# Performance work log

Hardware: AMD Instinct MI355X
Metric: run time of the kernel (lower is better)

Reference implementation:

```python
import jax, jax.numpy as jnp
import numpy as np

B, T, C, K = 8, 2048, 1024, 128

def setup_inputs() -> dict:
    key = jax.random.key(0)
    k1, k2, k3, k4 = jax.random.split(key, 4)
    scale = 0.02
    return {
        "x": jax.random.normal(k1, (B, T, C), dtype=jnp.float32),
        "Wq": jax.random.normal(k2, (C, K), dtype=jnp.float32) * scale,
        "Wk": jax.random.normal(k3, (C, K), dtype=jnp.float32) * scale,
        "Wv": jax.random.normal(k4, (C, K), dtype=jnp.float32) * scale,
    }

def reference(x, Wq, Wk, Wv):
    # Single-head causal self-attention (ModulUwagi.forward)
    q = jnp.einsum('btc,ck->btk', x, Wq)  # [B,T,K]
    k = jnp.einsum('btc,ck->btk', x, Wk)
    v = jnp.einsum('btc,ck->btk', x, Wv)
    hd = q.shape[-1]
    wei = jnp.einsum('btk,bsk->bts', q, k) * (hd ** -0.5)  # [B,T,T]
    causal = jnp.tril(jnp.ones((x.shape[1], x.shape[1]), dtype=bool))
    wei = jnp.where(causal, wei, -jnp.inf)
    wei = jax.nn.softmax(wei, axis=-1)
    out = jnp.einsum('bts,bsk->btk', wei, v)  # [B,T,K]
    return out
```

## Files before the change

kernel.cpp:

```cpp
#include <hip/hip_runtime.h>
#include <cmath>

#define Bn 8
#define Tn 2048
#define Cn 1024
#define Kn 128

typedef __attribute__((ext_vector_type(8))) short short8;
typedef __attribute__((ext_vector_type(4))) float f32x4;
typedef unsigned short u16;
typedef unsigned int u32;

#define NEGINF (-__builtin_huge_valf())

__device__ __forceinline__ u16 f2b(float f) {
    u32 u = __float_as_uint(f);
    u32 r = (u + 0x7FFFu + ((u >> 16) & 1u)) >> 16;
    return (u16)r;
}
__device__ __forceinline__ float b2f(u16 v) {
    u32 u = ((u32)v) << 16;
    return __uint_as_float(u);
}
__device__ __forceinline__ u32 cvtpk(float lo, float hi) {
    u32 r;
    asm("v_cvt_pk_bf16_f32 %0, %1, %2" : "=v"(r) : "v"(lo), "v"(hi));
    return r;
}

__device__ __forceinline__ void load_lds16(const u16* g, u16* l) {
    __builtin_amdgcn_global_load_lds(
        (const __attribute__((address_space(1))) u32*)(g),
        (__attribute__((address_space(3))) u32*)(l), 16, 0, 0);
}

__global__ __launch_bounds__(256)
void prep_kernel(const float* __restrict__ Wq, const float* __restrict__ Wk,
                 const float* __restrict__ Wv, u16* __restrict__ Wt)
{
    int id = blockIdx.x * 256 + threadIdx.x;
    int w   = id >> 15;
    int rem = id & 32767;
    int c   = rem >> 5;
    int n4  = (rem & 31) << 2;
    const float* W = (w == 0) ? Wq : (w == 1) ? Wk : Wv;
    float4 v = *(const float4*)(W + (size_t)c * Kn + n4);
    u16* dst = Wt + (size_t)w * Kn * Cn;
    dst[(size_t)(n4 + 0) * Cn + c] = f2b(v.x);
    dst[(size_t)(n4 + 1) * Cn + c] = f2b(v.y);
    dst[(size_t)(n4 + 2) * Cn + c] = f2b(v.z);
    dst[(size_t)(n4 + 3) * Cn + c] = f2b(v.w);
}

__global__ __launch_bounds__(256)
void proj3_kernel(const float* __restrict__ x, const u16* __restrict__ Wt,
                  u16* __restrict__ qkv)
{
    const int bid = blockIdx.x;
    const int g8  = bid >> 3, xr = bid & 7;
    const int w   = g8 % 3;
    const int rt  = (g8 / 3) * 8 + xr;
    const u16* wtg = Wt + (size_t)w * Kn * Cn;
    u16* outp = qkv + (size_t)w * Bn * Tn * Kn;
    const int row0 = rt * 128;
    const int tid  = threadIdx.x;
    const int lane = tid & 63;
    const int wid  = tid >> 6;
    const int l15  = lane & 15, lh = lane >> 4;
    const int m0 = (wid >> 1) * 64, n0 = (wid & 1) * 64;

    __shared__ u16 lds[32768];

    auto stageW = [&](int kk, int buf) {
        #pragma unroll
        for (int i = 0; i < 4; ++i) {
            int u = tid + i * 256;
            int n = u >> 3, c8 = u & 7;
            load_lds16(wtg + (size_t)n * Cn + kk + ((c8 ^ (n & 7)) << 3),
                       lds + 16384 + buf * 8192 + u * 8);
        }
    };
    auto loadX = [&](int kk, float4* xr4) {
        #pragma unroll
        for (int i = 0; i < 4; ++i) {
            int u = tid + i * 256;
            int r = u >> 3, c8 = u & 7;
            const float* s = x + (size_t)(row0 + r) * Cn + kk + c8 * 8;
            xr4[2 * i]     = *(const float4*)(s);
            xr4[2 * i + 1] = *(const float4*)(s + 4);
        }
    };
    auto writeX = [&](int buf, const float4* xr4) {
        u16* dst = lds + buf * 8192;
        #pragma unroll
        for (int i = 0; i < 4; ++i) {
            int u = tid + i * 256;
            int r = u >> 3, c8 = u & 7;
            uint4 pk;
            pk.x = cvtpk(xr4[2 * i].x,     xr4[2 * i].y);
            pk.y = cvtpk(xr4[2 * i].z,     xr4[2 * i].w);
            pk.z = cvtpk(xr4[2 * i + 1].x, xr4[2 * i + 1].y);
            pk.w = cvtpk(xr4[2 * i + 1].z, xr4[2 * i + 1].w);
            *(uint4*)(dst + r * 64 + ((c8 ^ (r & 7)) << 3)) = pk;
        }
    };

    f32x4 acc[4][4];
    #pragma unroll
    for (int i = 0; i < 4; ++i)
        #pragma unroll
        for (int j = 0; j < 4; ++j) acc[i][j] = (f32x4){0.f, 0.f, 0.f, 0.f};

    float4 xcur[8];
    loadX(0, xcur);
    stageW(0, 0);
    writeX(0, xcur);

    for (int step = 0; step < 16; ++step) {
        const int buf = step & 1;
        __syncthreads();
        const bool nxt = (step < 15);
        float4 xnext[8];
        if (nxt) {
            loadX((step + 1) * 64, xnext);
            stageW((step + 1) * 64, buf ^ 1);
        }
        const u16* Xb = lds + buf * 8192;
        const u16* Wb = lds + 16384 + buf * 8192;
        #pragma unroll
        for (int kc = 0; kc < 2; ++kc) {
            short8 af[4], bf[4];
            #pragma unroll
            for (int mg = 0; mg < 4; ++mg) {
                int row = m0 + mg * 16 + l15;
                int ch  = (kc * 4 + lh) ^ (row & 7);
                af[mg] = *(const short8*)(Xb + row * 64 + ch * 8);
            }
            #pragma unroll
            for (int ng = 0; ng < 4; ++ng) {
                int n  = n0 + ng * 16 + l15;
                int ch = (kc * 4 + lh) ^ (n & 7);
                bf[ng] = *(const short8*)(Wb + n * 64 + ch * 8);
            }
            #pragma unroll
            for (int mg = 0; mg < 4; ++mg)
                #pragma unroll
                for (int ng = 0; ng < 4; ++ng)
                    acc[mg][ng] = __builtin_amdgcn_mfma_f32_16x16x32_bf16(
                        af[mg], bf[ng], acc[mg][ng], 0, 0, 0);
        }
        if (nxt) writeX(buf ^ 1, xnext);
    }

    #pragma unroll
    for (int mg = 0; mg < 4; ++mg)
        #pragma unroll
        for (int ng = 0; ng < 4; ++ng)
            #pragma unroll
            for (int r = 0; r < 4; ++r) {
                int m = row0 + m0 + mg * 16 + lh * 4 + r;
                int n = n0 + ng * 16 + l15;
                outp[(size_t)m * Kn + n] = f2b(acc[mg][ng][r]);
            }
}

__device__ const int g_job_qi[32] = {0, 1,1, 2,2,2, 3,3,3,3, 4,4,4,4,
                                     5,5,5,5,5, 6,6,6,6,6,6, 7,7,7,7,7,7,7};
__device__ const int g_sup_b[32] = {0, 0,4, 0,4,8, 0,4,8,12, 0,5,10,15,
                                    0,4,9,14,19, 0,4,9,14,18,23, 0,4,9,13,18,22,27};
__device__ const int g_sup_e[32] = {4, 4,8, 4,8,12, 4,8,12,16, 5,10,15,20,
                                    4,9,14,19,24, 4,9,14,18,23,28, 4,9,13,18,22,27,32};

__global__ __launch_bounds__(512, 2)
void attn_kernel(const u16* __restrict__ qg_, const u16* __restrict__ kg_,
                 const u16* __restrict__ vg_, u16* __restrict__ pO,
                 float* __restrict__ pM, float* __restrict__ pL)
{
    const int b   = blockIdx.x;
    const int job = blockIdx.y;
    const int qi  = g_job_qi[job];
    const int sb  = g_sup_b[job], se = g_sup_e[job];

    const u16* qw = qg_ + (size_t)b * Tn * Kn;
    const u16* kw = kg_ + (size_t)b * Tn * Kn;
    const u16* vw = vg_ + (size_t)b * Tn * Kn;

    const int tid  = threadIdx.x;
    const int lane = tid & 63;
    const int wid  = tid >> 6;
    const int l15  = lane & 15, lh = lane >> 4;

    const int q0 = qi * 256 + wid * 32;
    const int qmax_w = q0 + 31;

    __shared__ u16 lds[32768];

    short8 qf[2][4];
    #pragma unroll
    for (int g = 0; g < 2; ++g)
        #pragma unroll
        for (int kc = 0; kc < 4; ++kc)
            qf[g][kc] = *(const short8*)(qw + (size_t)(q0 + g * 16 + l15) * Kn
                                         + kc * 32 + lh * 8);

    f32x4 acc[8][2];
    #pragma unroll
    for (int dt = 0; dt < 8; ++dt)
        #pragma unroll
        for (int g = 0; g < 2; ++g) acc[dt][g] = (f32x4){0.f, 0.f, 0.f, 0.f};
    float m_g[2] = {NEGINF, NEGINF}, l_g[2] = {0.f, 0.f};

    const float scale = 0.08838834764831843f;

    auto stageK = [&](int sup, int buf) {
        const u16* src = kw + (size_t)sup * 64 * Kn;
        u16* dst = lds + buf * 8192;
        #pragma unroll
        for (int i = 0; i < 2; ++i) {
            int u = wid * 128 + i * 64 + lane;
            int row = u >> 4;
            int c16 = (u & 15) ^ (row & 7);
            load_lds16(src + (size_t)row * Kn + c16 * 8,
                       dst + (size_t)(wid * 128 + i * 64) * 8);
        }
    };
    auto loadV = [&](int sup, uint4* vr) {
        const u16* src = vw + (size_t)sup * 64 * Kn;
        #pragma unroll
        for (int r = 0; r < 2; ++r) {
            int s  = tid & 63;
            int u8 = (tid >> 6) + 8 * r;
            vr[r] = *(const uint4*)(src + (size_t)s * Kn + u8 * 8);
        }
    };
    auto writeV = [&](int buf, const uint4* vr) {
        u16* dst = lds + 16384 + buf * 8192;
        #pragma unroll
        for (int r = 0; r < 2; ++r) {
            int s  = tid & 63;
            int u8 = (tid >> 6) + 8 * r;
            const u16* e = (const u16*)&vr[r];
            #pragma unroll
            for (int j = 0; j < 8; ++j) {
                int d = u8 * 8 + j;
                dst[d * 64 + (((s >> 3) ^ j) << 3) + (s & 7)] = e[j];
            }
        }
    };

    uint4 vreg[2];
    stageK(sb, 0);
    loadV(sb, vreg);
    writeV(0, vreg);

    for (int sup = sb; sup < se; ++sup) {
        const int cur = (sup - sb) & 1;
        __syncthreads();
        const bool have_next = (sup + 1 < se);
        if (have_next) {
            stageK(sup + 1, cur ^ 1);
            loadV(sup + 1, vreg);
        }
        if (sup * 64 <= qmax_w) {
            const u16* Kb = lds + cur * 8192;
            const u16* Vb = lds + 16384 + cur * 8192;
            f32x4 sf[4][2];
            #pragma unroll
            for (int mt = 0; mt < 4; ++mt)
                #pragma unroll
                for (int g = 0; g < 2; ++g) sf[mt][g] = (f32x4){0.f,0.f,0.f,0.f};
            #pragma unroll
            for (int kc = 0; kc < 4; ++kc) {
                short8 a[4];
                #pragma unroll
                for (int mt = 0; mt < 4; ++mt) {
                    int row = mt * 16 + l15;
                    int ch  = (kc * 4 + lh) ^ (row & 7);
                    a[mt] = *(const short8*)(Kb + row * 128 + ch * 8);
                }
                #pragma unroll
                for (int mt = 0; mt < 4; ++mt)
                    #pragma unroll
                    for (int g = 0; g < 2; ++g)
                        sf[mt][g] = __builtin_amdgcn_mfma_f32_16x16x32_bf16(
                            a[mt], qf[g][kc], sf[mt][g], 0, 0, 0);
            }
            const int sbase = sup * 64;
            u32 upk[2][4][2];
            float alpha_g[2];
            #pragma unroll
            for (int g = 0; g < 2; ++g) {
                const int qg = q0 + g * 16 + l15;
                float pv[16];
                float pm = NEGINF;
                #pragma unroll
                for (int mt = 0; mt < 4; ++mt)
                    #pragma unroll
                    for (int r = 0; r < 4; ++r) {
                        int sg = sbase + mt * 16 + lh * 4 + r;
                        float vv = sf[mt][g][r] * scale;
                        vv = (sg > qg) ? NEGINF : vv;
                        pv[mt * 4 + r] = vv;
                        pm = fmaxf(pm, vv);
                    }
                pm = fmaxf(pm, __shfl_xor(pm, 16));
                pm = fmaxf(pm, __shfl_xor(pm, 32));
                float mn  = fmaxf(m_g[g], pm);
                float mns = (mn == NEGINF) ? 0.f : mn;
                float al  = __expf(m_g[g] - mns);
                m_g[g] = mn;
                alpha_g[g] = al;
                float ps = 0.f;
                #pragma unroll
                for (int i = 0; i < 16; ++i) { pv[i] = __expf(pv[i] - mns); ps += pv[i]; }
                ps += __shfl_xor(ps, 16);
                ps += __shfl_xor(ps, 32);
                l_g[g] = l_g[g] * al + ps;
                #pragma unroll
                for (int mt = 0; mt < 4; ++mt)
                    #pragma unroll
                    for (int h = 0; h < 2; ++h)
                        upk[g][mt][h] = (u32)f2b(pv[mt * 4 + 2 * h])
                                      | ((u32)f2b(pv[mt * 4 + 2 * h + 1]) << 16);
            }
            #pragma unroll
            for (int dt = 0; dt < 8; ++dt)
                #pragma unroll
                for (int g = 0; g < 2; ++g)
                    acc[dt][g] *= alpha_g[g];
            #pragma unroll
            for (int ks = 0; ks < 2; ++ks) {
                short8 pf[2];
                #pragma unroll
                for (int g = 0; g < 2; ++g) {
                    union { u32 w[4]; short8 v; } uu;
                    #pragma unroll
                    for (int hp = 0; hp < 4; ++hp) {
                        int srcLane = l15 + 16 * ((lh & 1) * 2 + (hp >> 1));
                        u32 vA = __shfl(upk[g][2 * ks][hp & 1], srcLane, 64);
                        u32 vB = __shfl(upk[g][2 * ks + 1][hp & 1], srcLane, 64);
                        uu.w[hp] = (lh < 2) ? vA : vB;
                    }
                    pf[g] = uu.v;
                }
                #pragma unroll
                for (int dt = 0; dt < 8; ++dt) {
                    int d  = dt * 16 + l15;
                    int ch = (ks * 4 + lh) ^ (d & 7);
                    short8 av = *(const short8*)(Vb + d * 64 + ch * 8);
                    #pragma unroll
                    for (int g = 0; g < 2; ++g)
                        acc[dt][g] = __builtin_amdgcn_mfma_f32_16x16x32_bf16(
                            av, pf[g], acc[dt][g], 0, 0, 0);
                }
            }
        }
        if (have_next) writeV(cur ^ 1, vreg);
    }

    const size_t slotrow = ((size_t)b * 32 + job) * 256 + wid * 32;
    #pragma unroll
    for (int g = 0; g < 2; ++g) {
        size_t row = slotrow + g * 16 + l15;
        #pragma unroll
        for (int dt = 0; dt < 8; ++dt) {
            ushort4 o = { f2b(acc[dt][g][0]), f2b(acc[dt][g][1]),
                          f2b(acc[dt][g][2]), f2b(acc[dt][g][3]) };
            *(ushort4*)(pO + row * 128 + dt * 16 + lh * 4) = o;
        }
        if (lh == 0) {
            pM[row] = m_g[g];
            pL[row] = l_g[g];
        }
    }
}

__device__ const int g_cnt[8] = {1, 2, 3, 4, 4, 5, 6, 7};
__device__ const int g_s0[8]  = {0, 1, 3, 6, 10, 14, 19, 25};

__global__ __launch_bounds__(256)
void merge_kernel(const u16* __restrict__ pO, const float* __restrict__ pM,
                  const float* __restrict__ pL, float* __restrict__ out)
{
    const int bid = blockIdx.x;
    const int b   = bid >> 8;
    const int rem = bid & 255;
    const int qi  = rem >> 5;
    const int rg  = rem & 31;
    const int c = g_cnt[qi], s0 = g_s0[qi];
    const int tid = threadIdx.x;
    const int r8 = tid >> 5;
    const int dg = tid & 31;

    const int row = rg * 8 + r8;
    const size_t base = ((size_t)b * 32 + s0) * 256 + row;

    float mv[8];
    float M = NEGINF;
    #pragma unroll
    for (int i = 0; i < 8; ++i)
        if (i < c) { mv[i] = pM[base + (size_t)i * 256]; M = fmaxf(M, mv[i]); }
    float L = 0.f, w[8];
    #pragma unroll
    for (int i = 0; i < 8; ++i)
        if (i < c) {
            float e = __expf(mv[i] - M);
            L += pL[base + (size_t)i * 256] * e;
            w[i] = e;
        }
    const float invL = 1.f / L;

    float4 o = {0.f, 0.f, 0.f, 0.f};
    #pragma unroll
    for (int i = 0; i < 8; ++i)
        if (i < c) {
            ushort4 p = *(const ushort4*)(pO + (base + (size_t)i * 256) * 128 + dg * 4);
            float wi = w[i] * invL;
            o.x = fmaf(wi, b2f(p.x), o.x);
            o.y = fmaf(wi, b2f(p.y), o.y);
            o.z = fmaf(wi, b2f(p.z), o.z);
            o.w = fmaf(wi, b2f(p.w), o.w);
        }
    *(float4*)(out + ((size_t)b * Tn + qi * 256 + row) * Kn + dg * 4) = o;
}

extern "C" void kernel_launch(void* const* d_in, const int* in_sizes, int n_in,
                              void* d_out, int out_size, void* d_ws, size_t ws_size,
                              hipStream_t stream)
{
    const float* x  = (const float*)d_in[0];
    const float* Wq = (const float*)d_in[1];
    const float* Wk = (const float*)d_in[2];
    const float* Wv = (const float*)d_in[3];
    float* out = (float*)d_out;

    u16* ws = (u16*)d_ws;
    const size_t btk = (size_t)Bn * Tn * Kn;
    u16* q  = ws;
    u16* k  = ws + btk;
    u16* v  = ws + 2 * btk;
    u16* Wt = ws + 3 * btk;
    u16* pO = ws + 3 * btk + 393216;
    float* pM = (float*)(pO + (size_t)8388608);
    float* pL = pM + 65536;

    prep_kernel<<<384, 256, 0, stream>>>(Wq, Wk, Wv, Wt);
    proj3_kernel<<<384, 256, 0, stream>>>(x, Wt, ws);
    attn_kernel<<<dim3(Bn, 32), 512, 0, stream>>>(q, k, v, pO, pM, pL);
    merge_kernel<<<2048, 256, 0, stream>>>(pO, pM, pL, out);
}
```

Baseline: 71.80 us.

## Deepen projection pipeline with two-stage X register prefetch and manual waitcnt barriers

```diff
diff --git a/kernel.cpp b/kernel.cpp
--- a/kernel.cpp
+++ b/kernel.cpp
@@ -53,7 +53,7 @@
 }
 
 __global__ __launch_bounds__(256)
-void proj3_kernel(const float* __restrict__ x, const u16* __restrict__ Wt,
+void proj4_kernel(const float* __restrict__ x, const u16* __restrict__ Wt,
                   u16* __restrict__ qkv)
 {
     const int bid = blockIdx.x;
@@ -111,20 +111,7 @@
         #pragma unroll
         for (int j = 0; j < 4; ++j) acc[i][j] = (f32x4){0.f, 0.f, 0.f, 0.f};
 
-    float4 xcur[8];
-    loadX(0, xcur);
-    stageW(0, 0);
-    writeX(0, xcur);
-
-    for (int step = 0; step < 16; ++step) {
-        const int buf = step & 1;
-        __syncthreads();
-        const bool nxt = (step < 15);
-        float4 xnext[8];
-        if (nxt) {
-            loadX((step + 1) * 64, xnext);
-            stageW((step + 1) * 64, buf ^ 1);
-        }
+    auto compute = [&](int buf) {
         const u16* Xb = lds + buf * 8192;
         const u16* Wb = lds + 16384 + buf * 8192;
         #pragma unroll
@@ -149,7 +136,38 @@
                     acc[mg][ng] = __builtin_amdgcn_mfma_f32_16x16x32_bf16(
                         af[mg], bf[ng], acc[mg][ng], 0, 0, 0);
         }
-        if (nxt) writeX(buf ^ 1, xnext);
+    };
+
+    float4 xA[8], xB[8];
+    loadX(0, xA);
+    stageW(0, 0);
+    loadX(64, xB);
+    writeX(0, xA);
+    asm volatile("s_waitcnt vmcnt(8) lgkmcnt(0)" ::: "memory");
+    __builtin_amdgcn_sched_barrier(0);
+    __builtin_amdgcn_s_barrier();
+    __builtin_amdgcn_sched_barrier(0);
+
+    auto step = [&](int t, float4* XW, float4* XL) {
+        const int buf = t & 1;
+        if (t + 1 < 16) stageW((t + 1) * 64, buf ^ 1);
+        if (t + 2 < 16) loadX((t + 2) * 64, XL);
+        compute(buf);
+        if (t + 1 < 16) writeX(buf ^ 1, XW);
+        if (t < 15) {
+            if (t < 14)
+                asm volatile("s_waitcnt vmcnt(8) lgkmcnt(0)" ::: "memory");
+            else
+                asm volatile("s_waitcnt vmcnt(0) lgkmcnt(0)" ::: "memory");
+            __builtin_amdgcn_sched_barrier(0);
+            __builtin_amdgcn_s_barrier();
+            __builtin_amdgcn_sched_barrier(0);
+        }
+    };
+
+    for (int tt = 0; tt < 8; ++tt) {
+        step(2 * tt,     xB, xA);
+        step(2 * tt + 1, xA, xB);
     }
 
     #pragma unroll
@@ -445,7 +463,7 @@
     float* pL = pM + 65536;
 
     prep_kernel<<<384, 256, 0, stream>>>(Wq, Wk, Wv, Wt);
-    proj3_kernel<<<384, 256, 0, stream>>>(x, Wt, ws);
+    proj4_kernel<<<384, 256, 0, stream>>>(x, Wt, ws);
     attn_kernel<<<dim3(Bn, 32), 512, 0, stream>>>(q, k, v, pO, pM, pL);
     merge_kernel<<<2048, 256, 0, stream>>>(pO, pM, pL, out);
 }
```

After: 70.73 us. About the same (-1.5%).
